# Kernel tuning notes

Hardware: AMD Instinct MI355X
Metric: run time of the kernel (lower is better)

The kernel has to match this reference:

```python
import jax, jax.numpy as jnp
import numpy as np

GROUPS = 32
EPS = 1e-5
NUM_HEADS = 8
HEAD_DIM = 64
CHANNELS = 512


def group_norm(x, scale, bias):
    # x: [b, h, w, c]; normalize over (h, w, channels-within-group)
    b, h, w, c = x.shape
    xg = x.reshape(b, h, w, GROUPS, c // GROUPS)
    mean = jnp.mean(xg, axis=(1, 2, 4), keepdims=True)
    var = jnp.var(xg, axis=(1, 2, 4), keepdims=True)
    xg = (xg - mean) * jax.lax.rsqrt(var + EPS)
    return xg.reshape(b, h, w, c) * scale + bias


def setup_inputs() -> dict:
    key = jax.random.key(0)
    ks = jax.random.split(key, 8)
    b, hs, ws, c = 8, 32, 32, CHANNELS
    inner = NUM_HEADS * HEAD_DIM
    return {
        "x": jax.random.normal(ks[0], (b, hs, ws, c), dtype=jnp.float32),
        "t": jax.random.normal(ks[1], (b,), dtype=jnp.float32),
        "gn_scale": jnp.ones((c,), dtype=jnp.float32),
        "gn_bias": jnp.zeros((c,), dtype=jnp.float32),
        "w_qkv": jax.random.normal(ks[2], (c, 3 * inner), dtype=jnp.float32) * 0.02,
        "b_qkv": jnp.zeros((3 * inner,), dtype=jnp.float32),
        "w_out": jax.random.normal(ks[3], (inner, c), dtype=jnp.float32) * 0.02,
        "b_out": jnp.zeros((c,), dtype=jnp.float32),
    }


def reference(x, t, gn_scale, gn_bias, w_qkv, b_qkv, w_out, b_out):
    b, hs, ws, c = x.shape
    # NOTE: original reassigns x = GroupNorm(x); the residual uses the NORMALIZED x.
    xn = group_norm(x, gn_scale, gn_bias)
    x_flat = xn.reshape(b, hs * ws, c)                      # [b, s, c]
    qkv = x_flat @ w_qkv + b_qkv                            # [b, s, 3*nh*hd]
    qkv = qkv.reshape(b, hs * ws, NUM_HEADS, 3 * HEAD_DIM)
    q, k, v = jnp.split(qkv, 3, axis=-1)                    # each [b, s, nh, hd]
    q = q / jnp.sqrt(jnp.float32(HEAD_DIM))
    q = q.transpose(0, 2, 1, 3)                             # [b, nh, s, hd]
    k = k.transpose(0, 2, 1, 3)
    v = v.transpose(0, 2, 1, 3)
    attn = jax.nn.softmax(jnp.einsum('bhqd,bhkd->bhqk', q, k), axis=-1)
    out = jnp.einsum('bhqk,bhkd->bhqd', attn, v)            # [b, nh, s, hd]
    out = out.transpose(0, 2, 1, 3).reshape(b, hs * ws, NUM_HEADS * HEAD_DIM)
    h = out @ w_out + b_out                                 # [b, s, c]
    h = h.reshape(b, hs, ws, c)
    return xn + h
```

## Files before the change

kernel.cpp:

```cpp
#include <hip/hip_runtime.h>
#include <hip/hip_bf16.h>


#define B_    8
#define S_    1024
#define C_    512
#define NH    8
#define HD    64
#define QKVC  1536
#define GROUPS 32
#define GSIZE  16
#define EPSV   1e-5f
#define QSCL  0.18033688f

using frag8 = __attribute__((ext_vector_type(8))) short;
using f32x4 = __attribute__((ext_vector_type(4))) float;

__device__ __forceinline__ float bf2f(unsigned short u) {
    union { unsigned int i; float f; } v; v.i = ((unsigned int)u) << 16; return v.f;
}
__device__ __forceinline__ unsigned short f2bf(float f) {
    union { float f; unsigned int i; } v; v.f = f;
    unsigned int x = v.i;
    return (unsigned short)((x + 0x7fffu + ((x >> 16) & 1u)) >> 16);
}
__device__ __forceinline__ unsigned int pk2bf(float a, float b) {
    union { float f; unsigned int u; } x, y; x.f = a; y.f = b;
    return __builtin_amdgcn_perm(y.u + 0x8000u, x.u + 0x8000u, 0x07060302u);
}
__device__ __forceinline__ float fexp2(float x) {
#if __has_builtin(__builtin_amdgcn_exp2f)
    return __builtin_amdgcn_exp2f(x);
#else
    return exp2f(x);
#endif
}
__device__ __forceinline__ f32x4 zero4() {
    f32x4 z; z[0] = 0.f; z[1] = 0.f; z[2] = 0.f; z[3] = 0.f; return z;
}
__device__ __forceinline__ void gl_lds(const unsigned short* gp, unsigned short* lp) {
    __builtin_amdgcn_global_load_lds(
        (const __attribute__((address_space(1))) void*)gp,
        (__attribute__((address_space(3))) void*)lp, 16, 0, 0);
}

__global__ __launch_bounds__(256) void prep_kernel(
        const float* __restrict__ w_qkv, const float* __restrict__ w_out,
        unsigned short* __restrict__ wqkvT, unsigned short* __restrict__ woutT,
        const float* __restrict__ x,
        const float* __restrict__ scale, const float* __restrict__ bias,
        unsigned short* __restrict__ xn) {
    __shared__ unsigned short xcache[16384];
    __shared__ float s_red[8];
    int id = blockIdx.x;
    int t = threadIdx.x;
    if (id < 1024) {
        float* tile = (float*)xcache;
        const float* in; unsigned short* out; int N, n0, k0;
        if (id < 768) { in = w_qkv; out = wqkvT; N = QKVC; n0 = (id % 48) * 32; k0 = (id / 48) * 32; }
        else { int i2 = id - 768; in = w_out; out = woutT; N = C_; n0 = (i2 % 16) * 32; k0 = (i2 / 16) * 32; }
        for (int i = 0; i < 4; ++i) {
            int idx = t + i * 256; int r = idx >> 5, c = idx & 31;
            tile[r * 33 + c] = in[(size_t)(k0 + r) * N + n0 + c];
        }
        __syncthreads();
        for (int i = 0; i < 2; ++i) {
            int idx = t + i * 256;
            int r = idx >> 4, c2 = (idx & 15) * 2;
            unsigned int pk = pk2bf(tile[c2 * 33 + r], tile[(c2 + 1) * 33 + r]);
            *(unsigned int*)(&out[(size_t)(n0 + r) * C_ + k0 + c2]) = pk;
        }
        return;
    }
    int s = id - 1024;
    int xcd = s & 7, u = s >> 3;
    int gp = xcd * 16 + (u >> 1);
    int b = gp >> 4, g = ((gp & 15) << 1) | (u & 1);
    const float* xb = x + (size_t)b * S_ * C_;

    float sum = 0.f, ss = 0.f;
    for (int i = 0; i < 16; ++i) {
        int idx = t + i * 256;
        int row = idx >> 2, j = idx & 3;
        float4 v = *(const float4*)(xb + (size_t)row * C_ + g * GSIZE + j * 4);
        sum += v.x + v.y + v.z + v.w;
        ss  += v.x * v.x + v.y * v.y + v.z * v.z + v.w * v.w;
        uint2 c;
        c.x = pk2bf(v.x, v.y);
        c.y = pk2bf(v.z, v.w);
        *(uint2*)(&xcache[idx * 4]) = c;
    }
    for (int off = 1; off < 64; off <<= 1) {
        sum += __shfl_xor(sum, off);
        ss  += __shfl_xor(ss,  off);
    }
    int wid = t >> 6;
    if ((t & 63) == 0) { s_red[wid] = sum; s_red[4 + wid] = ss; }
    __syncthreads();
    sum = s_red[0] + s_red[1] + s_red[2] + s_red[3];
    ss  = s_red[4] + s_red[5] + s_red[6] + s_red[7];
    float mean = sum * (1.f / 16384.f);
    float var  = ss * (1.f / 16384.f) - mean * mean;
    float rinv = rsqrtf(var + EPSV);

    float sc[16], bi[16];
    for (int u2 = 0; u2 < 16; ++u2) {
        sc[u2] = scale[g * GSIZE + u2];
        bi[u2] = bias[g * GSIZE + u2];
    }
    for (int i = 0; i < 16; ++i) {
        int idx = t + i * 256;
        int row = idx >> 2, j = idx & 3;
        uint2 c = *(const uint2*)(&xcache[idx * 4]);
        float v0 = bf2f((unsigned short)(c.x & 0xffffu));
        float v1 = bf2f((unsigned short)(c.x >> 16));
        float v2 = bf2f((unsigned short)(c.y & 0xffffu));
        float v3 = bf2f((unsigned short)(c.y >> 16));
        int c0 = j * 4;
        float f0 = (v0 - mean) * rinv * sc[c0 + 0] + bi[c0 + 0];
        float f1 = (v1 - mean) * rinv * sc[c0 + 1] + bi[c0 + 1];
        float f2 = (v2 - mean) * rinv * sc[c0 + 2] + bi[c0 + 2];
        float f3 = (v3 - mean) * rinv * sc[c0 + 3] + bi[c0 + 3];
        uint2 o;
        o.x = pk2bf(f0, f1);
        o.y = pk2bf(f2, f3);
        *(uint2*)(xn + (size_t)b * S_ * C_ + (size_t)row * C_ + g * GSIZE + c0) = o;
    }
}

__global__ __launch_bounds__(256) void gemm_qkv_kernel(
        const unsigned short* __restrict__ A,
        const unsigned short* __restrict__ Bt,
        const float* __restrict__ bias,
        unsigned short* __restrict__ outA,
        unsigned short* __restrict__ outV) {
    __shared__ unsigned short As[2][128 * 32];
    __shared__ unsigned short Bs[2][128 * 32];
    unsigned int flat = blockIdx.y * 12u + blockIdx.x;
    unsigned int nid = (flat & 7u) * 96u + (flat >> 3);
    int my = nid / 12u, mx = nid % 12u;
    int m0 = my * 128, n0 = mx * 128;
    int t = threadIdx.x;
    int wid = t >> 6, lane = t & 63;
    int quad = lane >> 4, l16 = lane & 15;
    int wm = (wid >> 1) * 64, wn = (wid & 1) * 64;

    f32x4 acc[4][4];
    for (int mi = 0; mi < 4; ++mi)
        for (int ni = 0; ni < 4; ++ni) acc[mi][ni] = zero4();

    int srow = t >> 2;
    int sseg_sw = (t & 3) ^ ((t >> 3) & 3);
    auto stage = [&](int k0, int buf) {
        for (int i = 0; i < 2; ++i) {
            gl_lds(A + (size_t)(m0 + i * 64 + srow) * C_ + k0 + sseg_sw * 8,
                   &As[buf][(size_t)(i * 256 + wid * 64) * 8]);
            gl_lds(Bt + (size_t)(n0 + i * 64 + srow) * C_ + k0 + sseg_sw * 8,
                   &Bs[buf][(size_t)(i * 256 + wid * 64) * 8]);
        }
    };

    int rsw8 = ((l16 >> 1) & 3) * 8;

    stage(0, 0);
    const int nk = C_ >> 5;
    for (int i = 0; i < nk; ++i) {
        __syncthreads();
        if (i + 1 < nk) stage((i + 1) << 5, (i + 1) & 1);
        int buf = i & 1;

        frag8 bfrag[4], afrag[4];
        for (int ni = 0; ni < 4; ++ni)
            bfrag[ni] = *(const frag8*)(&Bs[buf][(wn + ni * 16 + l16) * 32 + ((quad * 8) ^ rsw8)]);
        for (int mi = 0; mi < 4; ++mi)
            afrag[mi] = *(const frag8*)(&As[buf][(wm + mi * 16 + l16) * 32 + ((quad * 8) ^ rsw8)]);

        for (int mi = 0; mi < 4; ++mi)
            for (int ni = 0; ni < 4; ++ni)
                acc[mi][ni] = __builtin_amdgcn_mfma_f32_16x16x32_bf16(
                    afrag[mi], bfrag[ni], acc[mi][ni], 0, 0, 0);
    }

    for (int ni = 0; ni < 4; ++ni) {
        int c0 = n0 + wn + ni * 16;
        float bv = bias[c0 + l16];
        int h = c0 / 192, rr = c0 % 192;
        if (rr >= 128) {
            int d = rr - 128 + l16;
            int bidx = m0 >> 10;
            unsigned short* vp = outV + (((size_t)bidx * NH + h) * HD + d) * S_
                               + (m0 & 1023) + wm + quad * 4;
            for (int mi = 0; mi < 4; ++mi) {
                uint2 pk;
                pk.x = pk2bf(acc[mi][ni][0] + bv, acc[mi][ni][1] + bv);
                pk.y = pk2bf(acc[mi][ni][2] + bv, acc[mi][ni][3] + bv);
                *(uint2*)(vp + mi * 16) = pk;
            }
        } else {
            float scl = (rr < 64) ? QSCL : 1.0f;
            int colk = h * 128 + rr + l16;
            for (int mi = 0; mi < 4; ++mi)
                for (int r = 0; r < 4; ++r) {
                    int row = m0 + wm + mi * 16 + quad * 4 + r;
                    outA[(size_t)row * 1024 + colk] = f2bf((acc[mi][ni][r] + bv) * scl);
                }
        }
    }
}

__global__ __launch_bounds__(256) void gemm_out_kernel(
        const unsigned short* __restrict__ A,
        const unsigned short* __restrict__ Bt,
        const float* __restrict__ bias,
        const unsigned short* __restrict__ resid,
        float* __restrict__ outF) {
    __shared__ unsigned short As[2][64 * 32];
    __shared__ unsigned short Bs[2][128 * 32];
    unsigned int flat = blockIdx.x;
    unsigned int nid = (flat & 7u) * 64u + (flat >> 3);
    int my = nid >> 2, mx = nid & 3;
    int m0 = my * 64, n0 = mx * 128;
    int t = threadIdx.x;
    int wid = t >> 6, lane = t & 63;
    int quad = lane >> 4, l16 = lane & 15;
    int wm = (wid >> 1) * 32, wn = (wid & 1) * 64;

    f32x4 acc[2][4];
    for (int mi = 0; mi < 2; ++mi)
        for (int ni = 0; ni < 4; ++ni) acc[mi][ni] = zero4();

    int srow = t >> 2;
    int sseg_sw = (t & 3) ^ ((t >> 3) & 3);
    auto stage = [&](int k0, int buf) {
        gl_lds(A + (size_t)(m0 + srow) * C_ + k0 + sseg_sw * 8,
               &As[buf][(size_t)wid * 512]);
        for (int i = 0; i < 2; ++i)
            gl_lds(Bt + (size_t)(n0 + i * 64 + srow) * C_ + k0 + sseg_sw * 8,
                   &Bs[buf][(size_t)(i * 256 + wid * 64) * 8]);
    };

    int rsw8 = ((l16 >> 1) & 3) * 8;

    stage(0, 0);
    const int nk = C_ >> 5;
    for (int i = 0; i < nk; ++i) {
        __syncthreads();
        if (i + 1 < nk) stage((i + 1) << 5, (i + 1) & 1);
        int buf = i & 1;

        frag8 bfrag[4], afrag[2];
        for (int ni = 0; ni < 4; ++ni)
            bfrag[ni] = *(const frag8*)(&Bs[buf][(wn + ni * 16 + l16) * 32 + ((quad * 8) ^ rsw8)]);
        for (int mi = 0; mi < 2; ++mi)
            afrag[mi] = *(const frag8*)(&As[buf][(wm + mi * 16 + l16) * 32 + ((quad * 8) ^ rsw8)]);

        for (int mi = 0; mi < 2; ++mi)
            for (int ni = 0; ni < 4; ++ni)
                acc[mi][ni] = __builtin_amdgcn_mfma_f32_16x16x32_bf16(
                    afrag[mi], bfrag[ni], acc[mi][ni], 0, 0, 0);
    }

    for (int ni = 0; ni < 4; ++ni) {
        int col = n0 + wn + ni * 16 + l16;
        float bv = bias[col];
        for (int mi = 0; mi < 2; ++mi)
            for (int r = 0; r < 4; ++r) {
                int row = m0 + wm + mi * 16 + quad * 4 + r;
                float v = acc[mi][ni][r] + bv + bf2f(resid[(size_t)row * C_ + col]);
                outF[(size_t)row * C_ + col] = v;
            }
    }
}

__global__ __launch_bounds__(256) void attn_kernel(
        const unsigned short* __restrict__ kq,
        const unsigned short* __restrict__ vT,
        unsigned short* __restrict__ attn_out) {
    int i = blockIdx.x;
    int xcd = i & 7, slot = i >> 3;
    int bh = xcd * 8 + (slot >> 3);
    int qt = slot & 7;
    int b = bh >> 3, h = bh & 7;

    int t = threadIdx.x;
    int wid = t >> 6, lane = t & 63, quad = lane >> 4, l16 = lane & 15;
    int q0 = qt * 128 + wid * 32;

    __shared__ unsigned short Ks[2][2][2048];
    __shared__ unsigned short Vs[2][2][2048];

    const unsigned short* qrow0 = kq + ((size_t)b * S_ + q0 + l16) * 1024 + h * 128;
    const unsigned short* qrow1 = qrow0 + (size_t)16 * 1024;
    frag8 qf[2][2];
    qf[0][0] = *(const frag8*)(qrow0 + quad * 8);
    qf[0][1] = *(const frag8*)(qrow0 + 32 + quad * 8);
    qf[1][0] = *(const frag8*)(qrow1 + quad * 8);
    qf[1][1] = *(const frag8*)(qrow1 + 32 + quad * 8);

    frag8 ones;
    for (int i2 = 0; i2 < 8; ++i2) ones[i2] = (short)0x3f80;

    f32x4 o[2][4], ol[2];
    for (int g = 0; g < 2; ++g) {
        ol[g] = zero4();
        for (int dt = 0; dt < 4; ++dt) o[g][dt] = zero4();
    }

    const unsigned short* kbase = kq + (size_t)b * S_ * 1024 + h * 128 + 64;
    const unsigned short* vbase = vT + ((size_t)b * NH + h) * HD * S_;

    int kdh = wid & 1, krh = wid >> 1;
    int krow = krh * 16 + (lane >> 2);
    int kseg = (lane & 3) ^ ((lane >> 3) & 3);
    int vd = wid * 16 + (lane >> 2);
    int vseg = lane & 3;
    int vkh = vseg >> 1, vsp = vseg & 1;
    int vsw = (lane >> 3) & 3;
    int vo1 = (((vsp * 2) ^ vsw) * 8) + vkh * 4;
    int vo2 = (((vsp * 2 + 1) ^ vsw) * 8) + vkh * 4;

    int ksw = (l16 >> 1) & 3;

    auto stageK = [&](int j0, int buf, int half) {
        gl_lds(kbase + (size_t)(j0 + krow) * 1024 + kdh * 32 + kseg * 8,
               &Ks[buf][half][kdh * 1024 + krh * 512]);
    };
    auto loadV = [&](int j0) {
        return *(const uint4*)(vbase + (size_t)vd * S_ + j0 + vseg * 8);
    };
    auto writeV = [&](uint4 w, int buf, int half) {
        unsigned short* vdst = &Vs[buf][half][vd * 32];
        uint2 g1; g1.x = w.x; g1.y = w.y;
        uint2 g2; g2.x = w.z; g2.y = w.w;
        *(uint2*)(vdst + vo1) = g1;
        *(uint2*)(vdst + vo2) = g2;
    };

    stageK(0, 0, 0);  stageK(32, 0, 1);
    writeV(loadV(0), 0, 0);  writeV(loadV(32), 0, 1);

    for (int it = 0; it < S_ / 64; ++it) {
        int cur = it & 1, nxt = cur ^ 1;
        __syncthreads();
        uint4 vn0, vn1;
        bool more = (it < S_ / 64 - 1);
        if (more) {
            int jn = (it + 1) * 64;
            stageK(jn, nxt, 0);
            stageK(jn + 32, nxt, 1);
            vn0 = loadV(jn);
            vn1 = loadV(jn + 32);
        }

        for (int half = 0; half < 2; ++half) {
            frag8 kf[2][2];
            for (int kh = 0; kh < 2; ++kh)
                for (int dh = 0; dh < 2; ++dh)
                    kf[kh][dh] = *(const frag8*)(&Ks[cur][half][dh * 1024
                        + (kh * 16 + l16) * 32 + ((quad ^ ksw) * 8)]);

            frag8 vf[4];
            for (int dt = 0; dt < 4; ++dt)
                vf[dt] = *(const frag8*)(&Vs[cur][half][(dt * 16 + l16) * 32
                        + ((quad ^ ksw) * 8)]);

            for (int g = 0; g < 2; ++g) {
                f32x4 s0 = zero4(), s1 = zero4();
                __builtin_amdgcn_s_setprio(1);
                s0 = __builtin_amdgcn_mfma_f32_16x16x32_bf16(kf[0][0], qf[g][0], s0, 0, 0, 0);
                s0 = __builtin_amdgcn_mfma_f32_16x16x32_bf16(kf[0][1], qf[g][1], s0, 0, 0, 0);
                s1 = __builtin_amdgcn_mfma_f32_16x16x32_bf16(kf[1][0], qf[g][0], s1, 0, 0, 0);
                s1 = __builtin_amdgcn_mfma_f32_16x16x32_bf16(kf[1][1], qf[g][1], s1, 0, 0, 0);
                __builtin_amdgcn_s_setprio(0);

                union { frag8 f; unsigned int u[4]; } pfu;
                pfu.u[0] = pk2bf(fexp2(s0[0]), fexp2(s0[1]));
                pfu.u[1] = pk2bf(fexp2(s0[2]), fexp2(s0[3]));
                pfu.u[2] = pk2bf(fexp2(s1[0]), fexp2(s1[1]));
                pfu.u[3] = pk2bf(fexp2(s1[2]), fexp2(s1[3]));

                __builtin_amdgcn_s_setprio(1);
                ol[g] = __builtin_amdgcn_mfma_f32_16x16x32_bf16(pfu.f, ones, ol[g], 0, 0, 0);
                for (int dt = 0; dt < 4; ++dt)
                    o[g][dt] = __builtin_amdgcn_mfma_f32_16x16x32_bf16(pfu.f, vf[dt], o[g][dt], 0, 0, 0);
                __builtin_amdgcn_s_setprio(0);
            }
        }

        if (more) {
            writeV(vn0, nxt, 0);
            writeV(vn1, nxt, 1);
        }
    }

    for (int g = 0; g < 2; ++g)
        for (int r = 0; r < 4; ++r) {
            float inv = 1.0f / ol[g][r];
            int qrw = q0 + g * 16 + quad * 4 + r;
            for (int dt = 0; dt < 4; ++dt) {
                int ch = h * HD + dt * 16 + l16;
                attn_out[((size_t)b * S_ + qrw) * C_ + ch] = f2bf(o[g][dt][r] * inv);
            }
        }
}

extern "C" void kernel_launch(void* const* d_in, const int* in_sizes, int n_in,
                              void* d_out, int out_size, void* d_ws, size_t ws_size,
                              hipStream_t stream) {
    const float* x        = (const float*)d_in[0];
    const float* gn_scale = (const float*)d_in[2];
    const float* gn_bias  = (const float*)d_in[3];
    const float* w_qkv    = (const float*)d_in[4];
    const float* b_qkv    = (const float*)d_in[5];
    const float* w_out    = (const float*)d_in[6];
    const float* b_out    = (const float*)d_in[7];
    float* out = (float*)d_out;

    char* ws = (char*)d_ws;
    unsigned short* xn    = (unsigned short*)(ws);
    unsigned short* kq    = (unsigned short*)(ws + ((size_t)8  << 20));
    unsigned short* attn  = (unsigned short*)(ws + ((size_t)24 << 20));
    unsigned short* vT    = (unsigned short*)(ws + ((size_t)32 << 20));
    unsigned short* wqkvT = (unsigned short*)(ws + ((size_t)40 << 20));
    unsigned short* woutT = (unsigned short*)(ws + ((size_t)40 << 20) + ((size_t)3 << 19));

    prep_kernel<<<dim3(1280), 256, 0, stream>>>(
        w_qkv, w_out, wqkvT, woutT, x, gn_scale, gn_bias, xn);

    gemm_qkv_kernel<<<dim3(QKVC / 128, (B_ * S_) / 128), 256, 0, stream>>>(
        xn, wqkvT, b_qkv, kq, vT);

    attn_kernel<<<dim3(512), 256, 0, stream>>>(kq, vT, attn);

    gemm_out_kernel<<<dim3(512), 256, 0, stream>>>(
        attn, woutT, b_out, xn, out);
}
```

Baseline: 149.9 us.

## Double K-step per barrier in out-proj GEMM; compute softmax row sums with VALU

The output projection GEMM now stages two 32-wide K slices per pipeline stage, so each barrier covers a 64-wide K chunk and the barrier count drops by half, at the cost of twice the LDS. In the attention kernel, the extra MFMA against a ones vector that produced softmax denominators is removed. Per-lane bf16 probabilities are summed with scalar adds and reduced across lanes with shuffles at the end. This trades one MFMA per tile for several VALU ops and some shuffles.

```diff
diff --git a/kernel.cpp b/kernel.cpp
--- a/kernel.cpp
+++ b/kernel.cpp
@@ -214,8 +214,8 @@
         const float* __restrict__ bias,
         const unsigned short* __restrict__ resid,
         float* __restrict__ outF) {
-    __shared__ unsigned short As[2][64 * 32];
-    __shared__ unsigned short Bs[2][128 * 32];
+    __shared__ unsigned short As[2][2][64 * 32];
+    __shared__ unsigned short Bs[2][2][128 * 32];
     unsigned int flat = blockIdx.x;
     unsigned int nid = (flat & 7u) * 64u + (flat >> 3);
     int my = nid >> 2, mx = nid & 3;
@@ -232,32 +232,36 @@
     int srow = t >> 2;
     int sseg_sw = (t & 3) ^ ((t >> 3) & 3);
     auto stage = [&](int k0, int buf) {
-        gl_lds(A + (size_t)(m0 + srow) * C_ + k0 + sseg_sw * 8,
-               &As[buf][(size_t)wid * 512]);
-        for (int i = 0; i < 2; ++i)
-            gl_lds(Bt + (size_t)(n0 + i * 64 + srow) * C_ + k0 + sseg_sw * 8,
-                   &Bs[buf][(size_t)(i * 256 + wid * 64) * 8]);
+        for (int s = 0; s < 2; ++s) {
+            gl_lds(A + (size_t)(m0 + srow) * C_ + k0 + s * 32 + sseg_sw * 8,
+                   &As[buf][s][(size_t)wid * 512]);
+            for (int i = 0; i < 2; ++i)
+                gl_lds(Bt + (size_t)(n0 + i * 64 + srow) * C_ + k0 + s * 32 + sseg_sw * 8,
+                       &Bs[buf][s][(size_t)(i * 256 + wid * 64) * 8]);
+        }
     };
 
     int rsw8 = ((l16 >> 1) & 3) * 8;
 
     stage(0, 0);
-    const int nk = C_ >> 5;
+    const int nk = C_ >> 6;
     for (int i = 0; i < nk; ++i) {
         __syncthreads();
-        if (i + 1 < nk) stage((i + 1) << 5, (i + 1) & 1);
+        if (i + 1 < nk) stage((i + 1) << 6, (i + 1) & 1);
         int buf = i & 1;
 
-        frag8 bfrag[4], afrag[2];
-        for (int ni = 0; ni < 4; ++ni)
-            bfrag[ni] = *(const frag8*)(&Bs[buf][(wn + ni * 16 + l16) * 32 + ((quad * 8) ^ rsw8)]);
-        for (int mi = 0; mi < 2; ++mi)
-            afrag[mi] = *(const frag8*)(&As[buf][(wm + mi * 16 + l16) * 32 + ((quad * 8) ^ rsw8)]);
-
-        for (int mi = 0; mi < 2; ++mi)
+        for (int s = 0; s < 2; ++s) {
+            frag8 bfrag[4], afrag[2];
             for (int ni = 0; ni < 4; ++ni)
-                acc[mi][ni] = __builtin_amdgcn_mfma_f32_16x16x32_bf16(
-                    afrag[mi], bfrag[ni], acc[mi][ni], 0, 0, 0);
+                bfrag[ni] = *(const frag8*)(&Bs[buf][s][(wn + ni * 16 + l16) * 32 + ((quad * 8) ^ rsw8)]);
+            for (int mi = 0; mi < 2; ++mi)
+                afrag[mi] = *(const frag8*)(&As[buf][s][(wm + mi * 16 + l16) * 32 + ((quad * 8) ^ rsw8)]);
+
+            for (int mi = 0; mi < 2; ++mi)
+                for (int ni = 0; ni < 4; ++ni)
+                    acc[mi][ni] = __builtin_amdgcn_mfma_f32_16x16x32_bf16(
+                        afrag[mi], bfrag[ni], acc[mi][ni], 0, 0, 0);
+        }
     }
 
     for (int ni = 0; ni < 4; ++ni) {
@@ -297,14 +301,10 @@
     qf[1][0] = *(const frag8*)(qrow1 + quad * 8);
     qf[1][1] = *(const frag8*)(qrow1 + 32 + quad * 8);
 
-    frag8 ones;
-    for (int i2 = 0; i2 < 8; ++i2) ones[i2] = (short)0x3f80;
-
-    f32x4 o[2][4], ol[2];
-    for (int g = 0; g < 2; ++g) {
-        ol[g] = zero4();
+    f32x4 o[2][4];
+    float lsum[2] = {0.f, 0.f};
+    for (int g = 0; g < 2; ++g)
         for (int dt = 0; dt < 4; ++dt) o[g][dt] = zero4();
-    }
 
     const unsigned short* kbase = kq + (size_t)b * S_ * 1024 + h * 128 + 64;
     const unsigned short* vbase = vT + ((size_t)b * NH + h) * HD * S_;
@@ -379,8 +379,17 @@
                 pfu.u[2] = pk2bf(fexp2(s1[0]), fexp2(s1[1]));
                 pfu.u[3] = pk2bf(fexp2(s1[2]), fexp2(s1[3]));
 
+                float lacc = 0.f;
+#pragma unroll
+                for (int w2 = 0; w2 < 4; ++w2) {
+                    union { unsigned int u; float f; } plo, phi;
+                    plo.u = pfu.u[w2] << 16;
+                    phi.u = pfu.u[w2] & 0xffff0000u;
+                    lacc += plo.f + phi.f;
+                }
+                lsum[g] += lacc;
+
                 __builtin_amdgcn_s_setprio(1);
-                ol[g] = __builtin_amdgcn_mfma_f32_16x16x32_bf16(pfu.f, ones, ol[g], 0, 0, 0);
                 for (int dt = 0; dt < 4; ++dt)
                     o[g][dt] = __builtin_amdgcn_mfma_f32_16x16x32_bf16(pfu.f, vf[dt], o[g][dt], 0, 0, 0);
                 __builtin_amdgcn_s_setprio(0);
@@ -393,15 +402,19 @@
         }
     }
 
-    for (int g = 0; g < 2; ++g)
+    for (int g = 0; g < 2; ++g) {
+        float lq = lsum[g];
+        lq += __shfl_xor(lq, 16);
+        lq += __shfl_xor(lq, 32);
         for (int r = 0; r < 4; ++r) {
-            float inv = 1.0f / ol[g][r];
+            float inv = 1.0f / __shfl(lq, quad * 4 + r);
             int qrw = q0 + g * 16 + quad * 4 + r;
             for (int dt = 0; dt < 4; ++dt) {
                 int ch = h * HD + dt * 16 + l16;
                 attn_out[((size_t)b * S_ + qrw) * C_ + ch] = f2bf(o[g][dt][r] * inv);
             }
         }
+    }
 }
 
 extern "C" void kernel_launch(void* const* d_in, const int* in_sizes, int n_in,
```

Result: no change. 147.9 us (-1.3%).
